# Kernel tuning notes

Hardware: AMD Instinct MI355X
Metric: run time of the kernel (lower is better)

Reference implementation:

```python
import jax, jax.numpy as jnp
import numpy as np

EPS = 1e-12  # torch F.normalize default eps
COMMITMENT_COST = 0.25

def l2_normalize(v, axis=-1):
    # matches torch.nn.functional.normalize(p=2): v / max(||v||, eps)
    n = jnp.linalg.norm(v, axis=axis, keepdims=True)
    return v / jnp.maximum(n, EPS)

def setup_inputs() -> dict:
    key = jax.random.key(0)
    k1, k2 = jax.random.split(key)
    N, D, K = 262144, 64, 1024
    x = jax.random.normal(k1, (N, D), dtype=jnp.float32)
    emb_weight = jax.random.normal(k2, (K, D), dtype=jnp.float32)
    return {"x": x, "emb_weight": emb_weight}

def reference(x, emb_weight):
    # x: [N, D] latents, emb_weight: [K, D] codebook
    xn = l2_normalize(x, axis=-1)                      # F.normalize(x, dim=-1)
    wn = l2_normalize(emb_weight, axis=-1)             # normalized codebook rows
    d2 = (jnp.sum(xn * xn, axis=-1, keepdims=True)
          + jnp.sum(wn * wn, axis=1)
          - 2.0 * jnp.matmul(xn, wn.T))                # [N, K]
    encoding_indices = jnp.argmin(d2, axis=1)          # [N]
    # quantize: normalize(embeddings(idx)) == wn[idx]
    quantized = wn[encoding_indices]                   # [N, D]
    q_latent_loss = jnp.mean((quantized - jax.lax.stop_gradient(xn)) ** 2)
    e_latent_loss = jnp.mean((xn - jax.lax.stop_gradient(quantized)) ** 2)
    loss = q_latent_loss + COMMITMENT_COST * e_latent_loss
    # straight-through estimator
    quantized_st = xn + jax.lax.stop_gradient(quantized - xn)
    return quantized_st, loss, encoding_indices
```

## Files before the change

kernel.cpp:

```cpp
#include <hip/hip_runtime.h>
#include <math.h>

#define N_ROWS 262144
#define DIM 64
#define K_CODES 1024
#define NT 64
#define ROWS_PER_BLOCK 128
#define EPSF 1e-12f

typedef _Float16 f16x8 __attribute__((ext_vector_type(8)));
typedef float f32x4 __attribute__((ext_vector_type(4)));


__global__ __launch_bounds__(64) void prep_codebook(
    const float* __restrict__ w, float* __restrict__ wn,
    float* __restrict__ msw, _Float16* __restrict__ wf)
{
    int k = blockIdx.x;
    int d = threadIdx.x;
    float v = w[k * DIM + d];
    float sq = v * v;
    #pragma unroll
    for (int off = 32; off; off >>= 1) sq += __shfl_xor(sq, off, 64);
    float n = fmaxf(sqrtf(sq), EPSF);
    float o = v / n;
    wn[k * DIM + d] = o;
    float s2 = o * o;
    #pragma unroll
    for (int off = 32; off; off >>= 1) s2 += __shfl_xor(s2, off, 64);
    if (d == 0) msw[k] = -0.5f * s2;

    _Float16 hi = (_Float16)o;
    _Float16 lo = (_Float16)(o - (float)hi);
    int t = k >> 4, nn = k & 15, s = d >> 5, g = (d >> 3) & 3, i = d & 7;
    size_t base = (size_t)t * 2048 + (size_t)s * 512 + (size_t)(g * 16 + nn) * 8 + i;
    wf[base] = hi;
    wf[base + 1024] = lo;
}

__global__ __launch_bounds__(256, 4) void vq_main_kernel(
    const float* __restrict__ x,
    const float* __restrict__ wn,
    const float* __restrict__ msw,
    const _Float16* __restrict__ wf,
    float* __restrict__ out_q,
    float* __restrict__ out_idx,
    float* __restrict__ partial)
{
    __shared__ float msw_lds[K_CODES + 16];
    __shared__ int idx_lds[ROWS_PER_BLOCK];
    __shared__ float inv_lds[ROWS_PER_BLOCK];
    __shared__ float red[4];

    const int tid = threadIdx.x;
    const int wv = tid >> 6;
    const int lane = tid & 63;
    const int nidx = lane & 15;
    const int g = lane >> 4;
    const int block_row0 = blockIdx.x * ROWS_PER_BLOCK;

    f16x8 ah[2][2], al[2][2];
    #pragma unroll
    for (int rt = 0; rt < 2; ++rt) {
        const int arow = block_row0 + wv * 32 + rt * 16 + nidx;
        const float* xrow = x + (size_t)arow * DIM + g * 8;
        float xv[2][8];
        #pragma unroll
        for (int s = 0; s < 2; ++s) {
            float4 q0 = *(const float4*)(xrow + s * 32);
            float4 q1 = *(const float4*)(xrow + s * 32 + 4);
            xv[s][0] = q0.x; xv[s][1] = q0.y; xv[s][2] = q0.z; xv[s][3] = q0.w;
            xv[s][4] = q1.x; xv[s][5] = q1.y; xv[s][6] = q1.z; xv[s][7] = q1.w;
        }
        float ss = 0.f;
        #pragma unroll
        for (int s = 0; s < 2; ++s)
            #pragma unroll
            for (int i = 0; i < 8; ++i) ss += xv[s][i] * xv[s][i];
        ss += __shfl_xor(ss, 16, 64);
        ss += __shfl_xor(ss, 32, 64);
        float nrm = fmaxf(sqrtf(ss), EPSF);
        float inv = 1.0f / nrm;
        if (g == 0) inv_lds[wv * 32 + rt * 16 + nidx] = inv;
        #pragma unroll
        for (int s = 0; s < 2; ++s)
            #pragma unroll
            for (int i = 0; i < 8; ++i) {
                float v = xv[s][i] * inv;
                _Float16 hi = (_Float16)v;
                ah[rt][s][i] = hi;
                al[rt][s][i] = (_Float16)(v - (float)hi);
            }
    }

    *(float4*)&msw_lds[tid * 4] = *(const float4*)(msw + tid * 4);
    if (tid < 4) {
        float4 z = {0.f, 0.f, 0.f, 0.f};
        *(float4*)&msw_lds[K_CODES + tid * 4] = z;
    }

    const _Float16* bbase = wf + (size_t)lane * 8;
    f16x8 cb0 = *(const f16x8*)(bbase);
    f16x8 cb1 = *(const f16x8*)(bbase + 512);
    f16x8 cb2 = *(const f16x8*)(bbase + 1024);
    f16x8 cb3 = *(const f16x8*)(bbase + 1536);
    float mval = msw[nidx];
    __syncthreads();

    float best[2][4];
    int bt[2][4];
    #pragma unroll
    for (int rt = 0; rt < 2; ++rt)
        #pragma unroll
        for (int r = 0; r < 4; ++r) { best[rt][r] = -3.4e38f; bt[rt][r] = 0; }

    for (int t = 0; t < NT; ++t) {
        const _Float16* np = bbase + (size_t)(t + 1) * 2048;
        f16x8 nb0 = *(const f16x8*)(np);
        f16x8 nb1 = *(const f16x8*)(np + 512);
        f16x8 nb2 = *(const f16x8*)(np + 1024);
        f16x8 nb3 = *(const f16x8*)(np + 1536);
        float nmval = msw_lds[(t + 1) * 16 + nidx];

        f32x4 acc0 = {mval, mval, mval, mval};
        f32x4 acc1 = {mval, mval, mval, mval};
        __builtin_amdgcn_s_setprio(1);
        acc0 = __builtin_amdgcn_mfma_f32_16x16x32_f16(ah[0][0], cb0, acc0, 0, 0, 0);
        acc1 = __builtin_amdgcn_mfma_f32_16x16x32_f16(ah[1][0], cb0, acc1, 0, 0, 0);
        acc0 = __builtin_amdgcn_mfma_f32_16x16x32_f16(ah[0][1], cb1, acc0, 0, 0, 0);
        acc1 = __builtin_amdgcn_mfma_f32_16x16x32_f16(ah[1][1], cb1, acc1, 0, 0, 0);
        acc0 = __builtin_amdgcn_mfma_f32_16x16x32_f16(al[0][0], cb0, acc0, 0, 0, 0);
        acc1 = __builtin_amdgcn_mfma_f32_16x16x32_f16(al[1][0], cb0, acc1, 0, 0, 0);
        acc0 = __builtin_amdgcn_mfma_f32_16x16x32_f16(al[0][1], cb1, acc0, 0, 0, 0);
        acc1 = __builtin_amdgcn_mfma_f32_16x16x32_f16(al[1][1], cb1, acc1, 0, 0, 0);
        acc0 = __builtin_amdgcn_mfma_f32_16x16x32_f16(ah[0][0], cb2, acc0, 0, 0, 0);
        acc1 = __builtin_amdgcn_mfma_f32_16x16x32_f16(ah[1][0], cb2, acc1, 0, 0, 0);
        acc0 = __builtin_amdgcn_mfma_f32_16x16x32_f16(ah[0][1], cb3, acc0, 0, 0, 0);
        acc1 = __builtin_amdgcn_mfma_f32_16x16x32_f16(ah[1][1], cb3, acc1, 0, 0, 0);
        __builtin_amdgcn_s_setprio(0);

        #pragma unroll
        for (int r = 0; r < 4; ++r) {
            if (acc0[r] > best[0][r]) { best[0][r] = acc0[r]; bt[0][r] = t; }
            if (acc1[r] > best[1][r]) { best[1][r] = acc1[r]; bt[1][r] = t; }
        }
        cb0 = nb0; cb1 = nb1; cb2 = nb2; cb3 = nb3; mval = nmval;
    }

    #pragma unroll
    for (int rt = 0; rt < 2; ++rt)
        #pragma unroll
        for (int r = 0; r < 4; ++r) {
            float b = best[rt][r];
            int bi = bt[rt][r] * 16 + nidx;
            #pragma unroll
            for (int off = 1; off <= 8; off <<= 1) {
                float ob = __shfl_xor(b, off, 64);
                int oi = __shfl_xor(bi, off, 64);
                if (ob > b || (ob == b && oi < bi)) { b = ob; bi = oi; }
            }
            if (nidx == 0)
                idx_lds[wv * 32 + rt * 16 + g * 4 + r] = bi;
        }
    __syncthreads();

    const int lr = tid >> 1;
    const int grow = block_row0 + lr;
    const int d0 = (tid & 1) * 32;
    const int ci = idx_lds[lr];
    const float invn = inv_lds[lr];
    const float4* xp = (const float4*)(x + (size_t)grow * DIM + d0);
    const float4* qp = (const float4*)(wn + (size_t)ci * DIM + d0);
    float4* op = (float4*)(out_q + (size_t)grow * DIM + d0);
    float ls = 0.f;
    #pragma unroll
    for (int i = 0; i < 8; ++i) {
        float4 qv = qp[i];
        float4 xv4 = xp[i];
        float e0 = qv.x - xv4.x * invn;
        float e1 = qv.y - xv4.y * invn;
        float e2 = qv.z - xv4.z * invn;
        float e3 = qv.w - xv4.w * invn;
        ls += e0 * e0 + e1 * e1 + e2 * e2 + e3 * e3;
        op[i] = qv;
    }
    if (!(tid & 1)) out_idx[grow] = (float)ci;

    float s = ls;
    #pragma unroll
    for (int off = 32; off; off >>= 1) s += __shfl_xor(s, off, 64);
    if (lane == 0) red[wv] = s;
    __syncthreads();
    if (tid == 0) partial[blockIdx.x] = (red[0] + red[1]) + (red[2] + red[3]);
}

__global__ __launch_bounds__(256) void finalize_kernel(
    const float* __restrict__ partial, float* __restrict__ loss_out)
{
    __shared__ float red[4];
    int t = threadIdx.x;
    float s = 0.f;
    #pragma unroll
    for (int i = 0; i < 8; ++i) s += partial[t * 8 + i];
    #pragma unroll
    for (int off = 32; off; off >>= 1) s += __shfl_xor(s, off, 64);
    if ((t & 63) == 0) red[t >> 6] = s;
    __syncthreads();
    if (t == 0)
        *loss_out = 1.25f * (((red[0] + red[1]) + (red[2] + red[3]))
                             / (float)((size_t)N_ROWS * DIM));
}

extern "C" void kernel_launch(void* const* d_in, const int* in_sizes, int n_in,
                              void* d_out, int out_size, void* d_ws, size_t ws_size,
                              hipStream_t stream) {
    const float* x = (const float*)d_in[0];
    const float* w = (const float*)d_in[1];
    float* out = (float*)d_out;
    float* ws = (float*)d_ws;

    float* wn      = ws;
    float* msw     = wn + (size_t)K_CODES * DIM;
    float* partial = msw + K_CODES;
    _Float16* wf   = (_Float16*)(partial + 2048);

    float* out_q    = out;
    float* out_loss = out + (size_t)N_ROWS * DIM;
    float* out_idx  = out_loss + 1;

    prep_codebook<<<K_CODES, 64, 0, stream>>>(w, wn, msw, wf);
    vq_main_kernel<<<N_ROWS / ROWS_PER_BLOCK, 256, 0, stream>>>(
        x, wn, msw, wf, out_q, out_idx, partial);
    finalize_kernel<<<1, 256, 0, stream>>>(partial, out_loss);
}
```

Measured before the change: 124.2 us.

## Deepen codebook prefetch to a four-stage register ring in the VQ loop

Replaces the single next-tile register prefetch of codebook fragments and norm terms with a four-deep rotating register buffer. Each tile's loads are now issued four tiles ahead, to hide global/L2 latency behind the MFMA work. Launch bounds drop from 4 to 3 blocks per SIMD so the extra VGPRs fit, which trades occupancy for prefetch depth. The LDS norm array padding grows so the lookahead reads stay in bounds, and codebook reads now run up to four tiles past the end of the buffer into workspace, though those values are never used.

```diff
diff --git a/kernel.cpp b/kernel.cpp
--- a/kernel.cpp
+++ b/kernel.cpp
@@ -38,7 +38,7 @@
     wf[base + 1024] = lo;
 }
 
-__global__ __launch_bounds__(256, 4) void vq_main_kernel(
+__global__ __launch_bounds__(256, 3) void vq_main_kernel(
     const float* __restrict__ x,
     const float* __restrict__ wn,
     const float* __restrict__ msw,
@@ -47,7 +47,7 @@
     float* __restrict__ out_idx,
     float* __restrict__ partial)
 {
-    __shared__ float msw_lds[K_CODES + 16];
+    __shared__ float msw_lds[K_CODES + 64];
     __shared__ int idx_lds[ROWS_PER_BLOCK];
     __shared__ float inv_lds[ROWS_PER_BLOCK];
     __shared__ float red[4];
@@ -94,17 +94,32 @@
     }
 
     *(float4*)&msw_lds[tid * 4] = *(const float4*)(msw + tid * 4);
-    if (tid < 4) {
+    if (tid < 16) {
         float4 z = {0.f, 0.f, 0.f, 0.f};
         *(float4*)&msw_lds[K_CODES + tid * 4] = z;
     }
 
     const _Float16* bbase = wf + (size_t)lane * 8;
-    f16x8 cb0 = *(const f16x8*)(bbase);
-    f16x8 cb1 = *(const f16x8*)(bbase + 512);
-    f16x8 cb2 = *(const f16x8*)(bbase + 1024);
-    f16x8 cb3 = *(const f16x8*)(bbase + 1536);
-    float mval = msw[nidx];
+    f16x8 S[4][4];
+    #pragma unroll
+    for (int q = 0; q < 4; ++q) {
+        const _Float16* tp = bbase + (size_t)q * 2048;
+        S[q][0] = *(const f16x8*)(tp);
+        S[q][1] = *(const f16x8*)(tp + 512);
+        S[q][2] = *(const f16x8*)(tp + 1024);
+        S[q][3] = *(const f16x8*)(tp + 1536);
+    }
+    float mv[4];
+    #pragma unroll
+    for (int q = 0; q < 4; ++q) mv[q] = msw[q * 16 + nidx];
+
+    const _Float16* p[4];
+    const float* mvp[4];
+    #pragma unroll
+    for (int q = 0; q < 4; ++q) {
+        p[q] = bbase + (size_t)(4 + q) * 2048;
+        mvp[q] = &msw_lds[(4 + q) * 16 + nidx];
+    }
     __syncthreads();
 
     float best[2][4];
@@ -114,37 +129,39 @@
         #pragma unroll
         for (int r = 0; r < 4; ++r) { best[rt][r] = -3.4e38f; bt[rt][r] = 0; }
 
-    for (int t = 0; t < NT; ++t) {
-        const _Float16* np = bbase + (size_t)(t + 1) * 2048;
-        f16x8 nb0 = *(const f16x8*)(np);
-        f16x8 nb1 = *(const f16x8*)(np + 512);
-        f16x8 nb2 = *(const f16x8*)(np + 1024);
-        f16x8 nb3 = *(const f16x8*)(np + 1536);
-        float nmval = msw_lds[(t + 1) * 16 + nidx];
-
-        f32x4 acc0 = {mval, mval, mval, mval};
-        f32x4 acc1 = {mval, mval, mval, mval};
-        __builtin_amdgcn_s_setprio(1);
-        acc0 = __builtin_amdgcn_mfma_f32_16x16x32_f16(ah[0][0], cb0, acc0, 0, 0, 0);
-        acc1 = __builtin_amdgcn_mfma_f32_16x16x32_f16(ah[1][0], cb0, acc1, 0, 0, 0);
-        acc0 = __builtin_amdgcn_mfma_f32_16x16x32_f16(ah[0][1], cb1, acc0, 0, 0, 0);
-        acc1 = __builtin_amdgcn_mfma_f32_16x16x32_f16(ah[1][1], cb1, acc1, 0, 0, 0);
-        acc0 = __builtin_amdgcn_mfma_f32_16x16x32_f16(al[0][0], cb0, acc0, 0, 0, 0);
-        acc1 = __builtin_amdgcn_mfma_f32_16x16x32_f16(al[1][0], cb0, acc1, 0, 0, 0);
-        acc0 = __builtin_amdgcn_mfma_f32_16x16x32_f16(al[0][1], cb1, acc0, 0, 0, 0);
-        acc1 = __builtin_amdgcn_mfma_f32_16x16x32_f16(al[1][1], cb1, acc1, 0, 0, 0);
-        acc0 = __builtin_amdgcn_mfma_f32_16x16x32_f16(ah[0][0], cb2, acc0, 0, 0, 0);
-        acc1 = __builtin_amdgcn_mfma_f32_16x16x32_f16(ah[1][0], cb2, acc1, 0, 0, 0);
-        acc0 = __builtin_amdgcn_mfma_f32_16x16x32_f16(ah[0][1], cb3, acc0, 0, 0, 0);
-        acc1 = __builtin_amdgcn_mfma_f32_16x16x32_f16(ah[1][1], cb3, acc1, 0, 0, 0);
-        __builtin_amdgcn_s_setprio(0);
-
-        #pragma unroll
-        for (int r = 0; r < 4; ++r) {
-            if (acc0[r] > best[0][r]) { best[0][r] = acc0[r]; bt[0][r] = t; }
-            if (acc1[r] > best[1][r]) { best[1][r] = acc1[r]; bt[1][r] = t; }
+    for (int it = 0; it < 16; ++it) {
+        #pragma unroll
+        for (int q = 0; q < 4; ++q) {
+            const int t = it * 4 + q;
+            f32x4 acc0 = {mv[q], mv[q], mv[q], mv[q]};
+            f32x4 acc1 = acc0;
+            __builtin_amdgcn_s_setprio(1);
+            acc0 = __builtin_amdgcn_mfma_f32_16x16x32_f16(ah[0][0], S[q][0], acc0, 0, 0, 0);
+            acc1 = __builtin_amdgcn_mfma_f32_16x16x32_f16(ah[1][0], S[q][0], acc1, 0, 0, 0);
+            acc0 = __builtin_amdgcn_mfma_f32_16x16x32_f16(ah[0][1], S[q][1], acc0, 0, 0, 0);
+            acc1 = __builtin_amdgcn_mfma_f32_16x16x32_f16(ah[1][1], S[q][1], acc1, 0, 0, 0);
+            acc0 = __builtin_amdgcn_mfma_f32_16x16x32_f16(al[0][0], S[q][0], acc0, 0, 0, 0);
+            acc1 = __builtin_amdgcn_mfma_f32_16x16x32_f16(al[1][0], S[q][0], acc1, 0, 0, 0);
+            acc0 = __builtin_amdgcn_mfma_f32_16x16x32_f16(al[0][1], S[q][1], acc0, 0, 0, 0);
+            acc1 = __builtin_amdgcn_mfma_f32_16x16x32_f16(al[1][1], S[q][1], acc1, 0, 0, 0);
+            acc0 = __builtin_amdgcn_mfma_f32_16x16x32_f16(ah[0][0], S[q][2], acc0, 0, 0, 0);
+            acc1 = __builtin_amdgcn_mfma_f32_16x16x32_f16(ah[1][0], S[q][2], acc1, 0, 0, 0);
+            acc0 = __builtin_amdgcn_mfma_f32_16x16x32_f16(ah[0][1], S[q][3], acc0, 0, 0, 0);
+            acc1 = __builtin_amdgcn_mfma_f32_16x16x32_f16(ah[1][1], S[q][3], acc1, 0, 0, 0);
+            __builtin_amdgcn_s_setprio(0);
+            S[q][0] = *(const f16x8*)(p[q]);
+            S[q][1] = *(const f16x8*)(p[q] + 512);
+            S[q][2] = *(const f16x8*)(p[q] + 1024);
+            S[q][3] = *(const f16x8*)(p[q] + 1536);
+            p[q] += 8192;
+            mv[q] = *mvp[q];
+            mvp[q] += 64;
+            #pragma unroll
+            for (int r = 0; r < 4; ++r) {
+                if (acc0[r] > best[0][r]) { best[0][r] = acc0[r]; bt[0][r] = t; }
+                if (acc1[r] > best[1][r]) { best[1][r] = acc1[r]; bt[1][r] = t; }
+            }
         }
-        cb0 = nb0; cb1 = nb1; cb2 = nb2; cb3 = nb3; mval = nmval;
     }
 
     #pragma unroll
```

Result: slower. 129.1 us (+3.9%).

## Split codebook across waves instead of rows, with cross-wave argmin merge

Applied to the files above, without the earlier changes.

Each block now handles 64 rows. All four waves hold the same 64 rows as A fragments, and each wave scans its own quarter of the codebook (256 codes) instead of the whole codebook for 32 rows. The tile loop is unrolled by two with double-buffered B registers, and per-wave best scores and indices are merged through shared memory. The aim is to cut codebook global loads per row and add MFMA independence, at the cost of more registers, lower occupancy (3 blocks), twice as many blocks and partials, and an extra LDS merge step.

```diff
diff --git a/kernel.cpp b/kernel.cpp
--- a/kernel.cpp
+++ b/kernel.cpp
@@ -4,8 +4,7 @@
 #define N_ROWS 262144
 #define DIM 64
 #define K_CODES 1024
-#define NT 64
-#define ROWS_PER_BLOCK 128
+#define ROWS_PER_BLOCK 64
 #define EPSF 1e-12f
 
 typedef _Float16 f16x8 __attribute__((ext_vector_type(8)));
@@ -38,7 +37,42 @@
     wf[base + 1024] = lo;
 }
 
-__global__ __launch_bounds__(256, 4) void vq_main_kernel(
+#define MFMA_(A, B, C) C = __builtin_amdgcn_mfma_f32_16x16x32_f16(A, B, C, 0, 0, 0)
+
+#define BODY(S0, S1, S2, S3, MV, PP, MVP, TL)                                 \
+  {                                                                           \
+    f32x4 a0 = {MV, MV, MV, MV};                                              \
+    f32x4 a1 = a0, a2 = a0, a3 = a0;                                          \
+    __builtin_amdgcn_s_setprio(1);                                            \
+    MFMA_(ah[0][0], S0, a0); MFMA_(ah[1][0], S0, a1);                         \
+    MFMA_(ah[2][0], S0, a2); MFMA_(ah[3][0], S0, a3);                         \
+    MFMA_(ah[0][1], S1, a0); MFMA_(ah[1][1], S1, a1);                         \
+    MFMA_(ah[2][1], S1, a2); MFMA_(ah[3][1], S1, a3);                         \
+    MFMA_(al[0][0], S0, a0); MFMA_(al[1][0], S0, a1);                         \
+    MFMA_(al[2][0], S0, a2); MFMA_(al[3][0], S0, a3);                         \
+    MFMA_(al[0][1], S1, a0); MFMA_(al[1][1], S1, a1);                         \
+    MFMA_(al[2][1], S1, a2); MFMA_(al[3][1], S1, a3);                         \
+    MFMA_(ah[0][0], S2, a0); MFMA_(ah[1][0], S2, a1);                         \
+    MFMA_(ah[2][0], S2, a2); MFMA_(ah[3][0], S2, a3);                         \
+    MFMA_(ah[0][1], S3, a0); MFMA_(ah[1][1], S3, a1);                         \
+    MFMA_(ah[2][1], S3, a2); MFMA_(ah[3][1], S3, a3);                         \
+    __builtin_amdgcn_s_setprio(0);                                            \
+    S0 = *(const f16x8*)(PP);                                                 \
+    S1 = *(const f16x8*)(PP + 512);                                           \
+    S2 = *(const f16x8*)(PP + 1024);                                          \
+    S3 = *(const f16x8*)(PP + 1536);                                          \
+    PP += 4096;                                                               \
+    MV = *MVP; MVP += 32;                                                     \
+    _Pragma("unroll")                                                         \
+    for (int r = 0; r < 4; ++r) {                                             \
+      if (a0[r] > best[0][r]) { best[0][r] = a0[r]; bt[0][r] = (TL); }        \
+      if (a1[r] > best[1][r]) { best[1][r] = a1[r]; bt[1][r] = (TL); }        \
+      if (a2[r] > best[2][r]) { best[2][r] = a2[r]; bt[2][r] = (TL); }        \
+      if (a3[r] > best[3][r]) { best[3][r] = a3[r]; bt[3][r] = (TL); }        \
+    }                                                                         \
+  }
+
+__global__ __launch_bounds__(256, 3) void vq_main_kernel(
     const float* __restrict__ x,
     const float* __restrict__ wn,
     const float* __restrict__ msw,
@@ -47,9 +81,11 @@
     float* __restrict__ out_idx,
     float* __restrict__ partial)
 {
-    __shared__ float msw_lds[K_CODES + 16];
-    __shared__ int idx_lds[ROWS_PER_BLOCK];
+    __shared__ float msw_lds[K_CODES + 32];
+    __shared__ float sc_w[4][ROWS_PER_BLOCK];
+    __shared__ int   id_w[4][ROWS_PER_BLOCK];
     __shared__ float inv_lds[ROWS_PER_BLOCK];
+    __shared__ int   idx_lds[ROWS_PER_BLOCK];
     __shared__ float red[4];
 
     const int tid = threadIdx.x;
@@ -59,10 +95,10 @@
     const int g = lane >> 4;
     const int block_row0 = blockIdx.x * ROWS_PER_BLOCK;
 
-    f16x8 ah[2][2], al[2][2];
-    #pragma unroll
-    for (int rt = 0; rt < 2; ++rt) {
-        const int arow = block_row0 + wv * 32 + rt * 16 + nidx;
+    f16x8 ah[4][2], al[4][2];
+    #pragma unroll
+    for (int rt = 0; rt < 4; ++rt) {
+        const int arow = block_row0 + rt * 16 + nidx;
         const float* xrow = x + (size_t)arow * DIM + g * 8;
         float xv[2][8];
         #pragma unroll
@@ -81,7 +117,7 @@
         ss += __shfl_xor(ss, 32, 64);
         float nrm = fmaxf(sqrtf(ss), EPSF);
         float inv = 1.0f / nrm;
-        if (g == 0) inv_lds[wv * 32 + rt * 16 + nidx] = inv;
+        if (wv == 0 && g == 0) inv_lds[rt * 16 + nidx] = inv;
         #pragma unroll
         for (int s = 0; s < 2; ++s)
             #pragma unroll
@@ -94,61 +130,42 @@
     }
 
     *(float4*)&msw_lds[tid * 4] = *(const float4*)(msw + tid * 4);
-    if (tid < 4) {
+    if (tid < 8) {
         float4 z = {0.f, 0.f, 0.f, 0.f};
         *(float4*)&msw_lds[K_CODES + tid * 4] = z;
     }
 
-    const _Float16* bbase = wf + (size_t)lane * 8;
-    f16x8 cb0 = *(const f16x8*)(bbase);
-    f16x8 cb1 = *(const f16x8*)(bbase + 512);
-    f16x8 cb2 = *(const f16x8*)(bbase + 1024);
-    f16x8 cb3 = *(const f16x8*)(bbase + 1536);
-    float mval = msw[nidx];
-    __syncthreads();
-
-    float best[2][4];
-    int bt[2][4];
-    #pragma unroll
-    for (int rt = 0; rt < 2; ++rt)
+    const _Float16* bbase = wf + (size_t)(wv * 16) * 2048 + (size_t)lane * 8;
+    f16x8 SA0 = *(const f16x8*)(bbase);
+    f16x8 SA1 = *(const f16x8*)(bbase + 512);
+    f16x8 SA2 = *(const f16x8*)(bbase + 1024);
+    f16x8 SA3 = *(const f16x8*)(bbase + 1536);
+    f16x8 SB0 = *(const f16x8*)(bbase + 2048);
+    f16x8 SB1 = *(const f16x8*)(bbase + 2560);
+    f16x8 SB2 = *(const f16x8*)(bbase + 3072);
+    f16x8 SB3 = *(const f16x8*)(bbase + 3584);
+    const _Float16* pA = bbase + 2 * 2048;
+    const _Float16* pB = bbase + 3 * 2048;
+    float mvA = msw[wv * 256 + nidx];
+    float mvB = msw[wv * 256 + 16 + nidx];
+    __syncthreads();
+    const float* mvpA = &msw_lds[wv * 256 + 32 + nidx];
+    const float* mvpB = &msw_lds[wv * 256 + 48 + nidx];
+
+    float best[4][4];
+    int bt[4][4];
+    #pragma unroll
+    for (int rt = 0; rt < 4; ++rt)
         #pragma unroll
         for (int r = 0; r < 4; ++r) { best[rt][r] = -3.4e38f; bt[rt][r] = 0; }
 
-    for (int t = 0; t < NT; ++t) {
-        const _Float16* np = bbase + (size_t)(t + 1) * 2048;
-        f16x8 nb0 = *(const f16x8*)(np);
-        f16x8 nb1 = *(const f16x8*)(np + 512);
-        f16x8 nb2 = *(const f16x8*)(np + 1024);
-        f16x8 nb3 = *(const f16x8*)(np + 1536);
-        float nmval = msw_lds[(t + 1) * 16 + nidx];
-
-        f32x4 acc0 = {mval, mval, mval, mval};
-        f32x4 acc1 = {mval, mval, mval, mval};
-        __builtin_amdgcn_s_setprio(1);
-        acc0 = __builtin_amdgcn_mfma_f32_16x16x32_f16(ah[0][0], cb0, acc0, 0, 0, 0);
-        acc1 = __builtin_amdgcn_mfma_f32_16x16x32_f16(ah[1][0], cb0, acc1, 0, 0, 0);
-        acc0 = __builtin_amdgcn_mfma_f32_16x16x32_f16(ah[0][1], cb1, acc0, 0, 0, 0);
-        acc1 = __builtin_amdgcn_mfma_f32_16x16x32_f16(ah[1][1], cb1, acc1, 0, 0, 0);
-        acc0 = __builtin_amdgcn_mfma_f32_16x16x32_f16(al[0][0], cb0, acc0, 0, 0, 0);
-        acc1 = __builtin_amdgcn_mfma_f32_16x16x32_f16(al[1][0], cb0, acc1, 0, 0, 0);
-        acc0 = __builtin_amdgcn_mfma_f32_16x16x32_f16(al[0][1], cb1, acc0, 0, 0, 0);
-        acc1 = __builtin_amdgcn_mfma_f32_16x16x32_f16(al[1][1], cb1, acc1, 0, 0, 0);
-        acc0 = __builtin_amdgcn_mfma_f32_16x16x32_f16(ah[0][0], cb2, acc0, 0, 0, 0);
-        acc1 = __builtin_amdgcn_mfma_f32_16x16x32_f16(ah[1][0], cb2, acc1, 0, 0, 0);
-        acc0 = __builtin_amdgcn_mfma_f32_16x16x32_f16(ah[0][1], cb3, acc0, 0, 0, 0);
-        acc1 = __builtin_amdgcn_mfma_f32_16x16x32_f16(ah[1][1], cb3, acc1, 0, 0, 0);
-        __builtin_amdgcn_s_setprio(0);
-
-        #pragma unroll
-        for (int r = 0; r < 4; ++r) {
-            if (acc0[r] > best[0][r]) { best[0][r] = acc0[r]; bt[0][r] = t; }
-            if (acc1[r] > best[1][r]) { best[1][r] = acc1[r]; bt[1][r] = t; }
-        }
-        cb0 = nb0; cb1 = nb1; cb2 = nb2; cb3 = nb3; mval = nmval;
-    }
-
-    #pragma unroll
-    for (int rt = 0; rt < 2; ++rt)
+    for (int it = 0; it < 8; ++it) {
+        BODY(SA0, SA1, SA2, SA3, mvA, pA, mvpA, it * 2)
+        BODY(SB0, SB1, SB2, SB3, mvB, pB, mvpB, it * 2 + 1)
+    }
+
+    #pragma unroll
+    for (int rt = 0; rt < 4; ++rt)
         #pragma unroll
         for (int r = 0; r < 4; ++r) {
             float b = best[rt][r];
@@ -159,14 +176,31 @@
                 int oi = __shfl_xor(bi, off, 64);
                 if (ob > b || (ob == b && oi < bi)) { b = ob; bi = oi; }
             }
-            if (nidx == 0)
-                idx_lds[wv * 32 + rt * 16 + g * 4 + r] = bi;
+            if (nidx == 0) {
+                const int row = rt * 16 + g * 4 + r;
+                sc_w[wv][row] = b;
+                id_w[wv][row] = wv * 256 + bi;
+            }
         }
     __syncthreads();
 
-    const int lr = tid >> 1;
+    if (tid < ROWS_PER_BLOCK) {
+        float bs = sc_w[0][tid];
+        int bid = id_w[0][tid];
+        #pragma unroll
+        for (int w = 1; w < 4; ++w) {
+            float s2 = sc_w[w][tid];
+            int i2 = id_w[w][tid];
+            if (s2 > bs) { bs = s2; bid = i2; }
+        }
+        idx_lds[tid] = bid;
+        out_idx[block_row0 + tid] = (float)bid;
+    }
+    __syncthreads();
+
+    const int lr = tid >> 2;
+    const int d0 = (tid & 3) * 16;
     const int grow = block_row0 + lr;
-    const int d0 = (tid & 1) * 32;
     const int ci = idx_lds[lr];
     const float invn = inv_lds[lr];
     const float4* xp = (const float4*)(x + (size_t)grow * DIM + d0);
@@ -174,7 +208,7 @@
     float4* op = (float4*)(out_q + (size_t)grow * DIM + d0);
     float ls = 0.f;
     #pragma unroll
-    for (int i = 0; i < 8; ++i) {
+    for (int i = 0; i < 4; ++i) {
         float4 qv = qp[i];
         float4 xv4 = xp[i];
         float e0 = qv.x - xv4.x * invn;
@@ -184,7 +218,6 @@
         ls += e0 * e0 + e1 * e1 + e2 * e2 + e3 * e3;
         op[i] = qv;
     }
-    if (!(tid & 1)) out_idx[grow] = (float)ci;
 
     float s = ls;
     #pragma unroll
@@ -201,7 +234,7 @@
     int t = threadIdx.x;
     float s = 0.f;
     #pragma unroll
-    for (int i = 0; i < 8; ++i) s += partial[t * 8 + i];
+    for (int i = 0; i < 16; ++i) s += partial[t * 16 + i];
     #pragma unroll
     for (int off = 32; off; off >>= 1) s += __shfl_xor(s, off, 64);
     if ((t & 63) == 0) red[t >> 6] = s;
@@ -222,7 +255,7 @@
     float* wn      = ws;
     float* msw     = wn + (size_t)K_CODES * DIM;
     float* partial = msw + K_CODES;
-    _Float16* wf   = (_Float16*)(partial + 2048);
+    _Float16* wf   = (_Float16*)(partial + 4096);
 
     float* out_q    = out;
     float* out_loss = out + (size_t)N_ROWS * DIM;
```

New measurement: 144.9 us. +16.7%, slower.

## Stage codebook tiles through double-buffered LDS instead of per-wave global loads

Applied to the files above, without the earlier changes.

Each block now loads every 16-code codebook tile once cooperatively into a double-buffered shared-memory buffer, with a register stage that prefetches two tiles ahead. All four waves read their B fragments from LDS instead of each wave fetching the same tile from global/L2. This cuts redundant global traffic but adds a block-wide barrier every tile iteration. Occupancy is raised from 4 to 5 blocks per SIMD, which limits register use.

```diff
diff --git a/kernel.cpp b/kernel.cpp
--- a/kernel.cpp
+++ b/kernel.cpp
@@ -38,7 +38,9 @@
     wf[base + 1024] = lo;
 }
 
-__global__ __launch_bounds__(256, 4) void vq_main_kernel(
+#define MFMA_(A, B, C) C = __builtin_amdgcn_mfma_f32_16x16x32_f16(A, B, C, 0, 0, 0)
+
+__global__ __launch_bounds__(256, 5) void vq_main_kernel(
     const float* __restrict__ x,
     const float* __restrict__ wn,
     const float* __restrict__ msw,
@@ -47,7 +49,8 @@
     float* __restrict__ out_idx,
     float* __restrict__ partial)
 {
-    __shared__ float msw_lds[K_CODES + 16];
+    __shared__ _Float16 bbuf[2][2048];
+    __shared__ float msw_lds[K_CODES];
     __shared__ int idx_lds[ROWS_PER_BLOCK];
     __shared__ float inv_lds[ROWS_PER_BLOCK];
     __shared__ float red[4];
@@ -94,17 +97,14 @@
     }
 
     *(float4*)&msw_lds[tid * 4] = *(const float4*)(msw + tid * 4);
-    if (tid < 4) {
-        float4 z = {0.f, 0.f, 0.f, 0.f};
-        *(float4*)&msw_lds[K_CODES + tid * 4] = z;
-    }
-
-    const _Float16* bbase = wf + (size_t)lane * 8;
-    f16x8 cb0 = *(const f16x8*)(bbase);
-    f16x8 cb1 = *(const f16x8*)(bbase + 512);
-    f16x8 cb2 = *(const f16x8*)(bbase + 1024);
-    f16x8 cb3 = *(const f16x8*)(bbase + 1536);
-    float mval = msw[nidx];
+
+    const _Float16* gsrc = wf + (size_t)tid * 8;
+    {
+        f16x8 s0 = *(const f16x8*)(gsrc);
+        *(f16x8*)&bbuf[0][tid * 8] = s0;
+    }
+    f16x8 stg = *(const f16x8*)(gsrc + 2048);
+    gsrc += 2 * 2048;
     __syncthreads();
 
     float best[2][4];
@@ -115,36 +115,39 @@
         for (int r = 0; r < 4; ++r) { best[rt][r] = -3.4e38f; bt[rt][r] = 0; }
 
     for (int t = 0; t < NT; ++t) {
-        const _Float16* np = bbase + (size_t)(t + 1) * 2048;
-        f16x8 nb0 = *(const f16x8*)(np);
-        f16x8 nb1 = *(const f16x8*)(np + 512);
-        f16x8 nb2 = *(const f16x8*)(np + 1024);
-        f16x8 nb3 = *(const f16x8*)(np + 1536);
-        float nmval = msw_lds[(t + 1) * 16 + nidx];
+        const int cur = t & 1;
+        const _Float16* bp = &bbuf[cur][lane * 8];
+        f16x8 b0 = *(const f16x8*)(bp);
+        f16x8 b1 = *(const f16x8*)(bp + 512);
+        f16x8 b2 = *(const f16x8*)(bp + 1024);
+        f16x8 b3 = *(const f16x8*)(bp + 1536);
+        float mval = msw_lds[t * 16 + nidx];
 
         f32x4 acc0 = {mval, mval, mval, mval};
-        f32x4 acc1 = {mval, mval, mval, mval};
+        f32x4 acc1 = acc0;
         __builtin_amdgcn_s_setprio(1);
-        acc0 = __builtin_amdgcn_mfma_f32_16x16x32_f16(ah[0][0], cb0, acc0, 0, 0, 0);
-        acc1 = __builtin_amdgcn_mfma_f32_16x16x32_f16(ah[1][0], cb0, acc1, 0, 0, 0);
-        acc0 = __builtin_amdgcn_mfma_f32_16x16x32_f16(ah[0][1], cb1, acc0, 0, 0, 0);
-        acc1 = __builtin_amdgcn_mfma_f32_16x16x32_f16(ah[1][1], cb1, acc1, 0, 0, 0);
-        acc0 = __builtin_amdgcn_mfma_f32_16x16x32_f16(al[0][0], cb0, acc0, 0, 0, 0);
-        acc1 = __builtin_amdgcn_mfma_f32_16x16x32_f16(al[1][0], cb0, acc1, 0, 0, 0);
-        acc0 = __builtin_amdgcn_mfma_f32_16x16x32_f16(al[0][1], cb1, acc0, 0, 0, 0);
-        acc1 = __builtin_amdgcn_mfma_f32_16x16x32_f16(al[1][1], cb1, acc1, 0, 0, 0);
-        acc0 = __builtin_amdgcn_mfma_f32_16x16x32_f16(ah[0][0], cb2, acc0, 0, 0, 0);
-        acc1 = __builtin_amdgcn_mfma_f32_16x16x32_f16(ah[1][0], cb2, acc1, 0, 0, 0);
-        acc0 = __builtin_amdgcn_mfma_f32_16x16x32_f16(ah[0][1], cb3, acc0, 0, 0, 0);
-        acc1 = __builtin_amdgcn_mfma_f32_16x16x32_f16(ah[1][1], cb3, acc1, 0, 0, 0);
+        MFMA_(ah[0][0], b0, acc0); MFMA_(ah[1][0], b0, acc1);
+        MFMA_(ah[0][1], b1, acc0); MFMA_(ah[1][1], b1, acc1);
+        MFMA_(al[0][0], b0, acc0); MFMA_(al[1][0], b0, acc1);
+        MFMA_(al[0][1], b1, acc0); MFMA_(al[1][1], b1, acc1);
+        MFMA_(ah[0][0], b2, acc0); MFMA_(ah[1][0], b2, acc1);
+        MFMA_(ah[0][1], b3, acc0); MFMA_(ah[1][1], b3, acc1);
         __builtin_amdgcn_s_setprio(0);
+
+        if (t + 1 < NT) {
+            *(f16x8*)&bbuf[cur ^ 1][tid * 8] = stg;
+            if (t + 2 < NT) {
+                stg = *(const f16x8*)(gsrc);
+                gsrc += 2048;
+            }
+        }
 
         #pragma unroll
         for (int r = 0; r < 4; ++r) {
             if (acc0[r] > best[0][r]) { best[0][r] = acc0[r]; bt[0][r] = t; }
             if (acc1[r] > best[1][r]) { best[1][r] = acc1[r]; bt[1][r] = t; }
         }
-        cb0 = nb0; cb1 = nb1; cb2 = nb2; cb3 = nb3; mval = nmval;
+        __syncthreads();
     }
 
     #pragma unroll
```

Result: faster. 120.2 us (-3.3%).
